# Kernel optimization log

Measured on AMD Instinct MI355X. Metric: run time of the kernel, lower is better.

The kernel has to match this reference:

```python
import jax, jax.numpy as jnp
import numpy as np

N_NODES = 50000
N_EDGES = 800000
D = 128
N_GRAPHS = 64


def setup_inputs() -> dict:
    key = jax.random.key(0)
    ks = jax.random.split(key, 10)
    x = jax.random.normal(ks[0], (N_NODES, D), dtype=jnp.float32)
    edge_weight = jax.random.uniform(ks[1], (N_EDGES,), dtype=jnp.float32)
    W1 = jax.random.normal(ks[2], (D, D), dtype=jnp.float32) / np.sqrt(D)
    b1 = jax.random.normal(ks[3], (D,), dtype=jnp.float32) * 0.01
    W2 = jax.random.normal(ks[4], (D, D), dtype=jnp.float32) / np.sqrt(D)
    b2 = jax.random.normal(ks[5], (D,), dtype=jnp.float32) * 0.01
    Wh = jax.random.normal(ks[6], (D, 1), dtype=jnp.float32) / np.sqrt(D)
    bh = jax.random.normal(ks[7], (1,), dtype=jnp.float32) * 0.01
    edge_index = jax.random.randint(ks[8], (2, N_EDGES), 0, N_NODES, dtype=jnp.int64)
    batch = jnp.sort(jax.random.randint(ks[9], (N_NODES,), 0, N_GRAPHS, dtype=jnp.int64))
    return {"x": x, "edge_weight": edge_weight, "W1": W1, "b1": b1,
            "W2": W2, "b2": b2, "Wh": Wh, "bh": bh,
            "edge_index": edge_index, "batch": batch}


def reference(x, edge_weight, W1, b1, W2, b2, Wh, bh, edge_index, batch):
    N = x.shape[0]
    # --- GCN normalization with self-loops (computed once; shared by layers) ---
    row, col = edge_index[0], edge_index[1]
    loop = jnp.arange(N, dtype=edge_index.dtype)
    row2 = jnp.concatenate([row, loop])   # source nodes
    col2 = jnp.concatenate([col, loop])   # target nodes
    ew2 = jnp.concatenate([edge_weight, jnp.ones((N,), dtype=x.dtype)])
    deg = jax.ops.segment_sum(ew2, col2, num_segments=N)
    dinv = jnp.where(deg > 0, jax.lax.rsqrt(deg), 0.0)
    norm = dinv[row2] * ew2 * dinv[col2]  # [E+N]

    def gcn_conv(h, W, b):
        h = h @ W                                   # [N, D_out]
        msg = norm[:, None] * h[row2]               # gather + scale, [E+N, D_out]
        return jax.ops.segment_sum(msg, col2, num_segments=N) + b

    # dropout is identity in eval mode
    h = jax.nn.relu(gcn_conv(x, W1, b1))
    h = jax.nn.relu(gcn_conv(h, W2, b2))

    # --- global mean pool over graphs ---
    counts = jax.ops.segment_sum(jnp.ones((N,), dtype=h.dtype), batch, num_segments=N_GRAPHS)
    pooled = jax.ops.segment_sum(h, batch, num_segments=N_GRAPHS)
    pooled = pooled / jnp.maximum(counts, 1.0)[:, None]
    return pooled @ Wh + bh
```

## Files before the change

### kernel.cpp

```cpp
#include <hip/hip_runtime.h>
#include <hip/hip_bf16.h>
#include <hip/hip_fp16.h>
#include <hip/hip_fp8.h>

#define N_NODES  50000
#define N_EDGES  800000
#define D        128
#define N_GRAPHS 64
#define CAP      64
#define EW_SCALE 1048576.0f
#define NB_GEMM1 391
#define NB_FILL  3125
#define NB_AGG16 3125

typedef _Float16 half8 __attribute__((ext_vector_type(8)));
typedef _Float16 half4 __attribute__((ext_vector_type(4)));
typedef float   float4v __attribute__((ext_vector_type(4)));
typedef float   f32x2   __attribute__((ext_vector_type(2)));

__device__ __forceinline__ float2 h2f(unsigned int u) {
    __half2 h = *reinterpret_cast<__half2*>(&u);
    return __half22float2(h);
}
__device__ __forceinline__ float hu2f(unsigned short u) {
    __half_raw hr; hr.x = u;
    return __half2float(__half(hr));
}
__device__ __forceinline__ float2 fp8x2_f32(unsigned short u) {
    f32x2 v = __builtin_amdgcn_cvt_pk_f32_fp8((int)u, false);
    return make_float2(v[0], v[1]);
}
__device__ __forceinline__ unsigned char f32_fp8(float f) {
    __hip_fp8_e4m3 q(f);
    return (unsigned char)q.__x;
}
__device__ __forceinline__ void unpack_pd(unsigned long long p, int& n, float& dv) {
    int c = (int)(p >> 40);
    n = c < CAP ? c : CAP;
    dv = rsqrtf(1.0f + (float)(p & 0xFFFFFFFFFFULL) * (1.0f / EW_SCALE));
}

__global__ __launch_bounds__(256) void fused_gemm1_fill(const float* __restrict__ X,
                                                        const float* __restrict__ W,
                                                        unsigned char* __restrict__ Y8,
                                                        const int* __restrict__ ei,
                                                        const float* __restrict__ ew,
                                                        unsigned long long* __restrict__ packed,
                                                        unsigned int* __restrict__ bucket) {
    __shared__ _Float16 Xs[128][72];
    __shared__ _Float16 Wt[128][72];

    if (blockIdx.x >= NB_GEMM1) {
        int e = (blockIdx.x - NB_GEMM1) * 256 + threadIdx.x;
        if (e >= N_EDGES) return;
        int r = ei[e];
        int c = ei[N_EDGES + e];
        float w = ew[e];
        unsigned long long add = (1ULL << 40) | (unsigned long long)(unsigned)(w * EW_SCALE + 0.5f);
        unsigned long long old = atomicAdd(&packed[c], add);
        unsigned pos = (unsigned)(old >> 40);
        if (pos < CAP) {
            unsigned short wh = __half_as_ushort(__float2half_rn(w));
            bucket[(size_t)c * CAP + pos] = (unsigned)r | ((unsigned)wh << 16);
        }
        return;
    }

    const int tid  = threadIdx.x;
    const int row0 = blockIdx.x * 128;
    const int wv   = tid >> 6;
    const int lane = tid & 63;
    const int quad = lane >> 4;
    const int l16  = lane & 15;

    float4v acc[8][2] = {};

    for (int kt = 0; kt < 4; kt++) {
        const int kbase = kt * 32;
        {
            int r  = tid >> 1;
            int rr = row0 + r; if (rr >= N_NODES) rr = N_NODES - 1;
            int k0 = (tid & 1) * 16;
            const float4* src = (const float4*)(X + (size_t)rr * 128 + kbase + k0);
#pragma unroll
            for (int i = 0; i < 4; i++) {
                float4 v = src[i];
                half4 hv;
                hv[0] = (_Float16)v.x; hv[1] = (_Float16)v.y;
                hv[2] = (_Float16)v.z; hv[3] = (_Float16)v.w;
                *(half4*)(&Xs[r][k0 + i * 4]) = hv;
            }
        }
        {
            int k  = tid >> 3;
            int c0 = (tid & 7) * 16;
            const float4* src = (const float4*)(W + (size_t)(kbase + k) * 128 + c0);
#pragma unroll
            for (int i = 0; i < 4; i++) {
                float4 v = src[i];
                Wt[c0 + i * 4 + 0][k] = (_Float16)v.x;
                Wt[c0 + i * 4 + 1][k] = (_Float16)v.y;
                Wt[c0 + i * 4 + 2][k] = (_Float16)v.z;
                Wt[c0 + i * 4 + 3][k] = (_Float16)v.w;
            }
        }
        __syncthreads();

        half8 b0 = *(const half8*)(&Wt[wv * 32 + l16][quad * 8]);
        half8 b1f = *(const half8*)(&Wt[wv * 32 + 16 + l16][quad * 8]);
#pragma unroll
        for (int rt = 0; rt < 8; rt++) {
            half8 a = *(const half8*)(&Xs[rt * 16 + l16][quad * 8]);
            acc[rt][0] = __builtin_amdgcn_mfma_f32_16x16x32_f16(a, b0,  acc[rt][0], 0, 0, 0);
            acc[rt][1] = __builtin_amdgcn_mfma_f32_16x16x32_f16(a, b1f, acc[rt][1], 0, 0, 0);
        }
        __syncthreads();
    }
#pragma unroll
    for (int rt = 0; rt < 8; rt++)
#pragma unroll
        for (int ct = 0; ct < 2; ct++)
#pragma unroll
            for (int r = 0; r < 4; r++) {
                int row = row0 + rt * 16 + quad * 4 + r;
                if (row < N_NODES)
                    Y8[(size_t)row * 128 + wv * 32 + ct * 16 + l16] = f32_fp8(acc[rt][ct][r]);
            }
}

__global__ __launch_bounds__(512) void agg1_gemm2_kernel(const unsigned char* __restrict__ x8in,
                                                         const unsigned long long* __restrict__ packed,
                                                         const unsigned int* __restrict__ bucket,
                                                         const float* __restrict__ b1,
                                                         const float* __restrict__ W2,
                                                         unsigned char* __restrict__ x2) {
    __shared__ _Float16 sh1[16][136];
    const int wv   = threadIdx.x >> 6;
    const int lane = threadIdx.x & 63;
    const unsigned short* xs16 = (const unsigned short*)x8in;
    const int node0 = blockIdx.x * 16;

    float2 bb = ((const float2*)b1)[lane];

    const int nodeA = node0 + wv * 2;
    const int nodeB = nodeA + 1;
    int nA; float dvA; unpack_pd(packed[nodeA], nA, dvA);
    int nB; float dvB; unpack_pd(packed[nodeB], nB, dvB);

    unsigned pkA = 0u, pkB = 0u;
    if (lane < nA) {
        unsigned eh = bucket[(size_t)nodeA * CAP + lane];
        int src = eh & 0xFFFFu;
        int sn; float sdv; unpack_pd(packed[src], sn, sdv);
        float v = hu2f((unsigned short)(eh >> 16)) * sdv;
        pkA = (unsigned)src | ((unsigned)__half_as_ushort(__float2half_rn(v)) << 16);
    }
    if (lane < nB) {
        unsigned eh = bucket[(size_t)nodeB * CAP + lane];
        int src = eh & 0xFFFFu;
        int sn; float sdv; unpack_pd(packed[src], sn, sdv);
        float v = hu2f((unsigned short)(eh >> 16)) * sdv;
        pkB = (unsigned)src | ((unsigned)__half_as_ushort(__float2half_rn(v)) << 16);
    }
    int pkiA = (int)pkA, pkiB = (int)pkB;

    float2 xsA = fp8x2_f32(xs16[(size_t)nodeA * 64 + lane]);
    float2 xsB = fp8x2_f32(xs16[(size_t)nodeB * 64 + lane]);
    float aAx = dvA * xsA.x, aAy = dvA * xsA.y;
    float aBx = dvB * xsB.x, aBy = dvB * xsB.y;

    int nmax = nA > nB ? nA : nB;
    for (int i = 0; i < nmax; i += 8) {
        unsigned av[8], bv[8];
#pragma unroll
        for (int j = 0; j < 8; j++) {
            av[j] = (unsigned)__shfl(pkiA, i + j);
            bv[j] = (unsigned)__shfl(pkiB, i + j);
        }
        unsigned short mA[8], mB[8];
#pragma unroll
        for (int j = 0; j < 8; j++) mA[j] = xs16[(size_t)(av[j] & 0xFFFFu) * 64 + lane];
#pragma unroll
        for (int j = 0; j < 8; j++) mB[j] = xs16[(size_t)(bv[j] & 0xFFFFu) * 64 + lane];
#pragma unroll
        for (int j = 0; j < 8; j++) {
            float2 f = fp8x2_f32(mA[j]);
            float v = hu2f((unsigned short)(av[j] >> 16));
            aAx += v * f.x; aAy += v * f.y;
        }
#pragma unroll
        for (int j = 0; j < 8; j++) {
            float2 f = fp8x2_f32(mB[j]);
            float v = hu2f((unsigned short)(bv[j] >> 16));
            aBx += v * f.x; aBy += v * f.y;
        }
    }

    float hAx = fmaxf(dvA * aAx + bb.x, 0.0f);
    float hAy = fmaxf(dvA * aAy + bb.y, 0.0f);
    float hBx = fmaxf(dvB * aBx + bb.x, 0.0f);
    float hBy = fmaxf(dvB * aBy + bb.y, 0.0f);
    sh1[wv * 2][lane * 2]         = (_Float16)hAx;
    sh1[wv * 2][lane * 2 + 1]     = (_Float16)hAy;
    sh1[wv * 2 + 1][lane * 2]     = (_Float16)hBx;
    sh1[wv * 2 + 1][lane * 2 + 1] = (_Float16)hBy;
    __syncthreads();

    const int quad = lane >> 4;
    const int l16  = lane & 15;
    float4v acc0 = {};
#pragma unroll
    for (int kc = 0; kc < 4; kc++) {
        const int k0 = kc * 32;
        half8 a = *(const half8*)(&sh1[l16][k0 + quad * 8]);
        const float* wp = W2 + (size_t)(k0 + quad * 8) * 128 + wv * 16 + l16;
        half8 b;
#pragma unroll
        for (int jj = 0; jj < 8; jj++) b[jj] = (_Float16)wp[jj * 128];
        acc0 = __builtin_amdgcn_mfma_f32_16x16x32_f16(a, b, acc0, 0, 0, 0);
    }
#pragma unroll
    for (int r = 0; r < 4; r++) {
        int row = node0 + quad * 4 + r;
        int rn; float s;
        unpack_pd(packed[row], rn, s);
        x2[(size_t)row * 128 + wv * 16 + l16] = f32_fp8(acc0[r] * s);
    }
}

__global__ __launch_bounds__(256) void agg_head_kernel(const unsigned char* __restrict__ x8,
                                                       const unsigned long long* __restrict__ packed,
                                                       const unsigned int* __restrict__ bucket,
                                                       const float* __restrict__ bias,
                                                       const float* __restrict__ Wh,
                                                       float* __restrict__ nodedot) {
    const int wv   = threadIdx.x >> 6;
    const int lane = threadIdx.x & 63;
    const unsigned short* xs16 = (const unsigned short*)x8;

    const int nodeA = blockIdx.x * 8 + wv * 2;
    const int nodeB = nodeA + 1;
    int nA; float dvA; unpack_pd(packed[nodeA], nA, dvA);
    int nB; float dvB; unpack_pd(packed[nodeB], nB, dvB);

    unsigned ehA = (lane < nA) ? bucket[(size_t)nodeA * CAP + lane] : 0u;
    unsigned ehB = (lane < nB) ? bucket[(size_t)nodeB * CAP + lane] : 0u;
    int eiA = (int)ehA, eiB = (int)ehB;

    float2 xsA = fp8x2_f32(xs16[(size_t)nodeA * 64 + lane]);
    float2 xsB = fp8x2_f32(xs16[(size_t)nodeB * 64 + lane]);
    float aAx = xsA.x, aAy = xsA.y;
    float aBx = xsB.x, aBy = xsB.y;

    int nmax = nA > nB ? nA : nB;
    for (int i = 0; i < nmax; i += 8) {
        unsigned av[8], bv[8];
#pragma unroll
        for (int j = 0; j < 8; j++) {
            av[j] = (unsigned)__shfl(eiA, i + j);
            bv[j] = (unsigned)__shfl(eiB, i + j);
        }
        unsigned short mA[8], mB[8];
#pragma unroll
        for (int j = 0; j < 8; j++) mA[j] = xs16[(size_t)(av[j] & 0xFFFFu) * 64 + lane];
#pragma unroll
        for (int j = 0; j < 8; j++) mB[j] = xs16[(size_t)(bv[j] & 0xFFFFu) * 64 + lane];
#pragma unroll
        for (int j = 0; j < 8; j++) {
            float2 f = fp8x2_f32(mA[j]);
            float v = hu2f((unsigned short)(av[j] >> 16));
            aAx += v * f.x; aAy += v * f.y;
        }
#pragma unroll
        for (int j = 0; j < 8; j++) {
            float2 f = fp8x2_f32(mB[j]);
            float v = hu2f((unsigned short)(bv[j] >> 16));
            aBx += v * f.x; aBy += v * f.y;
        }
    }

    float2 b = ((const float2*)bias)[lane];
    float2 w = ((const float2*)Wh)[lane];
    float hAx = fmaxf(dvA * aAx + b.x, 0.0f);
    float hAy = fmaxf(dvA * aAy + b.y, 0.0f);
    float hBx = fmaxf(dvB * aBx + b.x, 0.0f);
    float hBy = fmaxf(dvB * aBy + b.y, 0.0f);
    float sA = hAx * w.x + hAy * w.y;
    float sB = hBx * w.x + hBy * w.y;
#pragma unroll
    for (int off = 32; off > 0; off >>= 1) {
        sA += __shfl_down(sA, off, 64);
        sB += __shfl_down(sB, off, 64);
    }
    if (lane == 0) {
        nodedot[nodeA] = sA;
        nodedot[nodeB] = sB;
    }
}

__global__ __launch_bounds__(256) void final2_kernel(const float* __restrict__ nodedot,
                                                     const int* __restrict__ batch,
                                                     const float* __restrict__ bh,
                                                     float* __restrict__ out) {
    __shared__ float red[256];
    int g = blockIdx.x;
    int lo = 0, hi = N_NODES;
    while (lo < hi) { int mid = (lo + hi) >> 1; if (batch[mid] < g) lo = mid + 1; else hi = mid; }
    int a = lo;
    hi = N_NODES;
    while (lo < hi) { int mid = (lo + hi) >> 1; if (batch[mid] < g + 1) lo = mid + 1; else hi = mid; }
    int b = lo;

    float s = 0.0f;
    for (int n = a + threadIdx.x; n < b; n += 256) s += nodedot[n];
    red[threadIdx.x] = s;
    __syncthreads();
#pragma unroll
    for (int off = 128; off > 0; off >>= 1) {
        if (threadIdx.x < off) red[threadIdx.x] += red[threadIdx.x + off];
        __syncthreads();
    }
    if (threadIdx.x == 0)
        out[g] = red[0] / fmaxf((float)(b - a), 1.0f) + bh[0];
}

extern "C" void kernel_launch(void* const* d_in, const int* in_sizes, int n_in,
                              void* d_out, int out_size, void* d_ws, size_t ws_size,
                              hipStream_t stream) {
    const float* x   = (const float*)d_in[0];
    const float* ew  = (const float*)d_in[1];
    const float* W1  = (const float*)d_in[2];
    const float* b1  = (const float*)d_in[3];
    const float* W2  = (const float*)d_in[4];
    const float* b2  = (const float*)d_in[5];
    const float* Wh  = (const float*)d_in[6];
    const float* bh  = (const float*)d_in[7];
    const int*   ei  = (const int*)d_in[8];
    const int*   bat = (const int*)d_in[9];
    float* out = (float*)d_out;

    char* ws = (char*)d_ws;
    unsigned char* bufA8 = (unsigned char*)ws;            ws += (size_t)N_NODES * D;
    unsigned char* bufB8 = (unsigned char*)ws;            ws += (size_t)N_NODES * D;
    ws += 128 - ((size_t)ws & 127);
    unsigned int* bucket = (unsigned int*)ws;             ws += (size_t)N_NODES * CAP * 4;
    unsigned long long* packed = (unsigned long long*)ws; ws += (size_t)N_NODES * 8;
    float*  nodedot = (float*)ws;                         ws += (size_t)N_NODES * 4;

    const int nb_agg8 = N_NODES / 8;

    hipMemsetAsync(packed, 0, (size_t)N_NODES * 8, stream);

    fused_gemm1_fill<<<NB_GEMM1 + NB_FILL, 256, 0, stream>>>(x, W1, bufA8, ei, ew, packed, bucket);

    agg1_gemm2_kernel<<<NB_AGG16, 512, 0, stream>>>(bufA8, packed, bucket, b1, W2, bufB8);

    agg_head_kernel<<<nb_agg8, 256, 0, stream>>>(bufB8, packed, bucket, b2, Wh, nodedot);

    final2_kernel<<<N_GRAPHS, 256, 0, stream>>>(nodedot, bat, bh, out);
}
```

Before: 198.8 us.

## Split fp8 feature matrices into two 64-column planes for gather locality

```diff
diff --git a/kernel.cpp b/kernel.cpp
--- a/kernel.cpp
+++ b/kernel.cpp
@@ -12,23 +12,20 @@
 #define NB_GEMM1 391
 #define NB_FILL  3125
 #define NB_AGG16 3125
+#define PSTR     ((size_t)N_NODES * 64)
 
 typedef _Float16 half8 __attribute__((ext_vector_type(8)));
 typedef _Float16 half4 __attribute__((ext_vector_type(4)));
 typedef float   float4v __attribute__((ext_vector_type(4)));
 typedef float   f32x2   __attribute__((ext_vector_type(2)));
 
-__device__ __forceinline__ float2 h2f(unsigned int u) {
-    __half2 h = *reinterpret_cast<__half2*>(&u);
-    return __half22float2(h);
-}
 __device__ __forceinline__ float hu2f(unsigned short u) {
     __half_raw hr; hr.x = u;
     return __half2float(__half(hr));
 }
-__device__ __forceinline__ float2 fp8x2_f32(unsigned short u) {
+__device__ __forceinline__ float fp8_f32(unsigned char u) {
     f32x2 v = __builtin_amdgcn_cvt_pk_f32_fp8((int)u, false);
-    return make_float2(v[0], v[1]);
+    return v[0];
 }
 __device__ __forceinline__ unsigned char f32_fp8(float f) {
     __hip_fp8_e4m3 q(f);
@@ -123,8 +120,10 @@
 #pragma unroll
             for (int r = 0; r < 4; r++) {
                 int row = row0 + rt * 16 + quad * 4 + r;
+                int col = wv * 32 + ct * 16 + l16;
                 if (row < N_NODES)
-                    Y8[(size_t)row * 128 + wv * 32 + ct * 16 + l16] = f32_fp8(acc[rt][ct][r]);
+                    Y8[(size_t)(col >> 6) * PSTR + (size_t)row * 64 + (col & 63)] =
+                        f32_fp8(acc[rt][ct][r]);
             }
 }
 
@@ -137,10 +136,7 @@
     __shared__ _Float16 sh1[16][136];
     const int wv   = threadIdx.x >> 6;
     const int lane = threadIdx.x & 63;
-    const unsigned short* xs16 = (const unsigned short*)x8in;
     const int node0 = blockIdx.x * 16;
-
-    float2 bb = ((const float2*)b1)[lane];
 
     const int nodeA = node0 + wv * 2;
     const int nodeB = nodeA + 1;
@@ -163,47 +159,42 @@
         pkB = (unsigned)src | ((unsigned)__half_as_ushort(__float2half_rn(v)) << 16);
     }
     int pkiA = (int)pkA, pkiB = (int)pkB;
-
-    float2 xsA = fp8x2_f32(xs16[(size_t)nodeA * 64 + lane]);
-    float2 xsB = fp8x2_f32(xs16[(size_t)nodeB * 64 + lane]);
-    float aAx = dvA * xsA.x, aAy = dvA * xsA.y;
-    float aBx = dvB * xsB.x, aBy = dvB * xsB.y;
-
     int nmax = nA > nB ? nA : nB;
-    for (int i = 0; i < nmax; i += 8) {
-        unsigned av[8], bv[8];
-#pragma unroll
-        for (int j = 0; j < 8; j++) {
-            av[j] = (unsigned)__shfl(pkiA, i + j);
-            bv[j] = (unsigned)__shfl(pkiB, i + j);
-        }
-        unsigned short mA[8], mB[8];
-#pragma unroll
-        for (int j = 0; j < 8; j++) mA[j] = xs16[(size_t)(av[j] & 0xFFFFu) * 64 + lane];
-#pragma unroll
-        for (int j = 0; j < 8; j++) mB[j] = xs16[(size_t)(bv[j] & 0xFFFFu) * 64 + lane];
-#pragma unroll
-        for (int j = 0; j < 8; j++) {
-            float2 f = fp8x2_f32(mA[j]);
-            float v = hu2f((unsigned short)(av[j] >> 16));
-            aAx += v * f.x; aAy += v * f.y;
-        }
-#pragma unroll
-        for (int j = 0; j < 8; j++) {
-            float2 f = fp8x2_f32(mB[j]);
-            float v = hu2f((unsigned short)(bv[j] >> 16));
-            aBx += v * f.x; aBy += v * f.y;
-        }
-    }
-
-    float hAx = fmaxf(dvA * aAx + bb.x, 0.0f);
-    float hAy = fmaxf(dvA * aAy + bb.y, 0.0f);
-    float hBx = fmaxf(dvB * aBx + bb.x, 0.0f);
-    float hBy = fmaxf(dvB * aBy + bb.y, 0.0f);
-    sh1[wv * 2][lane * 2]         = (_Float16)hAx;
-    sh1[wv * 2][lane * 2 + 1]     = (_Float16)hAy;
-    sh1[wv * 2 + 1][lane * 2]     = (_Float16)hBx;
-    sh1[wv * 2 + 1][lane * 2 + 1] = (_Float16)hBy;
+
+    float hA[2], hB[2];
+#pragma unroll
+    for (int p = 0; p < 2; p++) {
+        const unsigned char* pl = x8in + (size_t)p * PSTR;
+        float aA = dvA * fp8_f32(pl[(size_t)nodeA * 64 + lane]);
+        float aB = dvB * fp8_f32(pl[(size_t)nodeB * 64 + lane]);
+        for (int i = 0; i < nmax; i += 8) {
+            unsigned av[8], bv[8];
+#pragma unroll
+            for (int j = 0; j < 8; j++) {
+                av[j] = (unsigned)__shfl(pkiA, i + j);
+                bv[j] = (unsigned)__shfl(pkiB, i + j);
+            }
+            unsigned char mA[8], mB[8];
+#pragma unroll
+            for (int j = 0; j < 8; j++) mA[j] = pl[(size_t)(av[j] & 0xFFFFu) * 64 + lane];
+#pragma unroll
+            for (int j = 0; j < 8; j++) mB[j] = pl[(size_t)(bv[j] & 0xFFFFu) * 64 + lane];
+#pragma unroll
+            for (int j = 0; j < 8; j++)
+                aA += hu2f((unsigned short)(av[j] >> 16)) * fp8_f32(mA[j]);
+#pragma unroll
+            for (int j = 0; j < 8; j++)
+                aB += hu2f((unsigned short)(bv[j] >> 16)) * fp8_f32(mB[j]);
+        }
+        float bb = b1[p * 64 + lane];
+        hA[p] = fmaxf(dvA * aA + bb, 0.0f);
+        hB[p] = fmaxf(dvB * aB + bb, 0.0f);
+    }
+
+    sh1[wv * 2][lane]          = (_Float16)hA[0];
+    sh1[wv * 2][64 + lane]     = (_Float16)hA[1];
+    sh1[wv * 2 + 1][lane]      = (_Float16)hB[0];
+    sh1[wv * 2 + 1][64 + lane] = (_Float16)hB[1];
     __syncthreads();
 
     const int quad = lane >> 4;
@@ -219,12 +210,14 @@
         for (int jj = 0; jj < 8; jj++) b[jj] = (_Float16)wp[jj * 128];
         acc0 = __builtin_amdgcn_mfma_f32_16x16x32_f16(a, b, acc0, 0, 0, 0);
     }
+    const int col = wv * 16 + l16;
+    unsigned char* x2p = x2 + (size_t)(col >> 6) * PSTR + (col & 63);
 #pragma unroll
     for (int r = 0; r < 4; r++) {
         int row = node0 + quad * 4 + r;
         int rn; float s;
         unpack_pd(packed[row], rn, s);
-        x2[(size_t)row * 128 + wv * 16 + l16] = f32_fp8(acc0[r] * s);
+        x2p[(size_t)row * 64] = f32_fp8(acc0[r] * s);
     }
 }
 
@@ -236,7 +229,6 @@
                                                        float* __restrict__ nodedot) {
     const int wv   = threadIdx.x >> 6;
     const int lane = threadIdx.x & 63;
-    const unsigned short* xs16 = (const unsigned short*)x8;
 
     const int nodeA = blockIdx.x * 8 + wv * 2;
     const int nodeB = nodeA + 1;
@@ -246,47 +238,39 @@
     unsigned ehA = (lane < nA) ? bucket[(size_t)nodeA * CAP + lane] : 0u;
     unsigned ehB = (lane < nB) ? bucket[(size_t)nodeB * CAP + lane] : 0u;
     int eiA = (int)ehA, eiB = (int)ehB;
-
-    float2 xsA = fp8x2_f32(xs16[(size_t)nodeA * 64 + lane]);
-    float2 xsB = fp8x2_f32(xs16[(size_t)nodeB * 64 + lane]);
-    float aAx = xsA.x, aAy = xsA.y;
-    float aBx = xsB.x, aBy = xsB.y;
-
     int nmax = nA > nB ? nA : nB;
-    for (int i = 0; i < nmax; i += 8) {
-        unsigned av[8], bv[8];
-#pragma unroll
-        for (int j = 0; j < 8; j++) {
-            av[j] = (unsigned)__shfl(eiA, i + j);
-            bv[j] = (unsigned)__shfl(eiB, i + j);
-        }
-        unsigned short mA[8], mB[8];
-#pragma unroll
-        for (int j = 0; j < 8; j++) mA[j] = xs16[(size_t)(av[j] & 0xFFFFu) * 64 + lane];
-#pragma unroll
-        for (int j = 0; j < 8; j++) mB[j] = xs16[(size_t)(bv[j] & 0xFFFFu) * 64 + lane];
-#pragma unroll
-        for (int j = 0; j < 8; j++) {
-            float2 f = fp8x2_f32(mA[j]);
-            float v = hu2f((unsigned short)(av[j] >> 16));
-            aAx += v * f.x; aAy += v * f.y;
-        }
-#pragma unroll
-        for (int j = 0; j < 8; j++) {
-            float2 f = fp8x2_f32(mB[j]);
-            float v = hu2f((unsigned short)(bv[j] >> 16));
-            aBx += v * f.x; aBy += v * f.y;
-        }
-    }
-
-    float2 b = ((const float2*)bias)[lane];
-    float2 w = ((const float2*)Wh)[lane];
-    float hAx = fmaxf(dvA * aAx + b.x, 0.0f);
-    float hAy = fmaxf(dvA * aAy + b.y, 0.0f);
-    float hBx = fmaxf(dvB * aBx + b.x, 0.0f);
-    float hBy = fmaxf(dvB * aBy + b.y, 0.0f);
-    float sA = hAx * w.x + hAy * w.y;
-    float sB = hBx * w.x + hBy * w.y;
+
+    float sA = 0.0f, sB = 0.0f;
+#pragma unroll
+    for (int p = 0; p < 2; p++) {
+        const unsigned char* pl = x8 + (size_t)p * PSTR;
+        float aA = fp8_f32(pl[(size_t)nodeA * 64 + lane]);
+        float aB = fp8_f32(pl[(size_t)nodeB * 64 + lane]);
+        for (int i = 0; i < nmax; i += 8) {
+            unsigned av[8], bv[8];
+#pragma unroll
+            for (int j = 0; j < 8; j++) {
+                av[j] = (unsigned)__shfl(eiA, i + j);
+                bv[j] = (unsigned)__shfl(eiB, i + j);
+            }
+            unsigned char mA[8], mB[8];
+#pragma unroll
+            for (int j = 0; j < 8; j++) mA[j] = pl[(size_t)(av[j] & 0xFFFFu) * 64 + lane];
+#pragma unroll
+            for (int j = 0; j < 8; j++) mB[j] = pl[(size_t)(bv[j] & 0xFFFFu) * 64 + lane];
+#pragma unroll
+            for (int j = 0; j < 8; j++)
+                aA += hu2f((unsigned short)(av[j] >> 16)) * fp8_f32(mA[j]);
+#pragma unroll
+            for (int j = 0; j < 8; j++)
+                aB += hu2f((unsigned short)(bv[j] >> 16)) * fp8_f32(mB[j]);
+        }
+        float bb = bias[p * 64 + lane];
+        float ww = Wh[p * 64 + lane];
+        sA += fmaxf(dvA * aA + bb, 0.0f) * ww;
+        sB += fmaxf(dvB * aB + bb, 0.0f) * ww;
+    }
+
 #pragma unroll
     for (int off = 32; off > 0; off >>= 1) {
         sA += __shfl_down(sA, off, 64);
```

Measured after the change: 231.4 us. 1.16x slower.
